# Optimization experiments

Measured on AMD Instinct MI355X. Metric: run time of the kernel, lower is better.

The kernel has to match this reference:

```python
import jax, jax.numpy as jnp
import numpy as np

NUM_HEADS = 16  # matches init_kwargs num_heads


def setup_inputs() -> dict:
    key = jax.random.key(0)
    k0, k1, k2, k3, k4 = jax.random.split(key, 5)
    B, p, C = 8, 64, 1024
    N = p * p
    s = 1.0 / np.sqrt(C).astype(np.float32)
    return {
        "x": jax.random.normal(k0, (B, 3, N, C), jnp.float32),
        "wq": jax.random.normal(k1, (C, C), jnp.float32) * s,
        "wk": jax.random.normal(k2, (C, C), jnp.float32) * s,
        "wv": jax.random.normal(k3, (C, C), jnp.float32) * s,
        "w_proj": jax.random.normal(k4, (C, C), jnp.float32) * s,
        "b_proj": jnp.zeros((C,), jnp.float32),
    }


def reference(x, wq, wk, wv, w_proj, b_proj):
    # x: [B, 3, N, C] triplane tokens, N = p*p
    B, G, N, C = x.shape
    p = int(round(N ** 0.5))
    H = NUM_HEADS
    d = C // H
    scale = d ** -0.5

    xg = x.reshape(B, 3, p, p, C)
    # Linear projections are pointwise, so project each plane element once
    # (the torch code redundantly projects gathered copies; math is identical).
    qh = (xg @ wq.T).reshape(B, 3, p, p, H, d)
    kh = (xg @ wk.T).reshape(B, 3, p, p, H, d)
    vh = (xg @ wv.T).reshape(B, 3, p, p, H, d)

    outs = []
    for i in range(3):  # fixed loop over the 3 planes
        q_i = qh[:, i]                       # [B, a, j, H, d] query pixel (a, j)
        k_yz = kh[:, (i + 1) % 3]            # keys: row a of next plane -> [B, a, k, H, d]
        v_yz = vh[:, (i + 1) % 3]
        k_zx = kh[:, (i + 2) % 3]            # keys: column j of other plane -> [B, k, j, H, d]
        v_zx = vh[:, (i + 2) % 3]
        # scores against the p row-keys and p column-keys (2p keys total, 1 query)
        s1 = jnp.einsum('bajhd,bakhd->bajhk', q_i, k_yz) * scale
        s2 = jnp.einsum('bajhd,bkjhd->bajhk', q_i, k_zx) * scale
        attn = jax.nn.softmax(jnp.concatenate([s1, s2], axis=-1), axis=-1)  # [B,a,j,H,2p]
        a1, a2 = attn[..., :p], attn[..., p:]
        o = (jnp.einsum('bajhk,bakhd->bajhd', a1, v_yz)
             + jnp.einsum('bajhk,bkjhd->bajhd', a2, v_zx))  # [B,a,j,H,d]
        outs.append(o.reshape(B, N, C))
    # torch buffer is filled in [plane, B, N] order then reinterpreted as [B,3,N];
    # replicate that reshape quirk faithfully.
    out = jnp.stack(outs, axis=0)            # [3, B, N, C]
    out = out @ w_proj.T + b_proj
    return out.reshape(B, 3, N, C)
```

## Files before the change

kernel.cpp:

```cpp
#include <hip/hip_runtime.h>
#include <hip/hip_bf16.h>
#include <stdint.h>
#include <type_traits>

typedef __hip_bfloat16 hbf16;
typedef short bf16x8 __attribute__((ext_vector_type(8)));
typedef float f32x4 __attribute__((ext_vector_type(4)));

#define MFMA16(a, b, c) __builtin_amdgcn_mfma_f32_16x16x32_bf16((a), (b), (c), 0, 0, 0)

__device__ __forceinline__ void gload_lds16(const void* g, void* l) {
  __builtin_amdgcn_global_load_lds(
      (const __attribute__((address_space(1))) void*)g,
      (__attribute__((address_space(3))) void*)l, 16, 0, 0);
}

__device__ __forceinline__ float b2f(unsigned short u) {
  union { unsigned int u32; float f; } cv;
  cv.u32 = ((unsigned int)u) << 16;
  return cv.f;
}
__device__ __forceinline__ unsigned short f2b(float f) {
  hbf16 h = __float2bfloat16(f);
  return __builtin_bit_cast(unsigned short, h);
}

__device__ __forceinline__ int swz(int row, int col) {
  return row * 64 + (col ^ ((row & 7) << 3));
}

__global__ __launch_bounds__(256) void cvt_f32_bf16(
    const float* __restrict__ src, unsigned short* __restrict__ dst, long long n)
{
  const long long i0 = ((long long)blockIdx.x * 256 + threadIdx.x) * 8;
  const long long stride = (long long)gridDim.x * 2048;
  for (long long i = i0; i < n; i += stride) {
    const float4 a = *(const float4*)(src + i);
    const float4 b = *(const float4*)(src + i + 4);
    bf16x8 o;
    o[0] = (short)f2b(a.x); o[1] = (short)f2b(a.y);
    o[2] = (short)f2b(a.z); o[3] = (short)f2b(a.w);
    o[4] = (short)f2b(b.x); o[5] = (short)f2b(b.y);
    o[6] = (short)f2b(b.z); o[7] = (short)f2b(b.w);
    *(bf16x8*)(dst + i) = o;
  }
}

template <typename OutT>
__global__ __launch_bounds__(512, 2) void gemm_bt(
    const unsigned short* __restrict__ A,
    const unsigned short* __restrict__ W,
    const float* __restrict__ bias,
    OutT* __restrict__ C,
    int M, int N, int K)
{
  __shared__ __attribute__((aligned(16))) unsigned short As[4][8192];
  __shared__ __attribute__((aligned(16))) unsigned short Bs[4][8192];

  const int tid   = threadIdx.x;
  const int lane  = tid & 63;
  const int w     = tid >> 6;
  const int wr128 = (w >> 2) * 128;
  const int wn64  = (w & 3) * 64;
  const int lr    = lane & 15;
  const int lg    = lane >> 4;
  const int wofs  = w * 512;

  const int nwg     = gridDim.x;
  const int bx      = blockIdx.x;
  const int logical = (bx & 7) * (nwg >> 3) + (bx >> 3);
  const int colsN   = N >> 8;
  const int tileM   = logical / colsN;
  const int tileN   = logical - tileM * colsN;
  const size_t rowBase = (size_t)tileM * 256;
  const int    colBase = tileN * 256;

  const int sRow   = tid >> 2;
  const int sChunk = (tid & 3) ^ ((tid >> 3) & 3);
  const unsigned short* Ag0 = A + (rowBase + sRow) * (size_t)K + sChunk * 8;
  const unsigned short* Ag1 = Ag0 + (size_t)128 * K;
  const unsigned short* Wg0 = W + ((size_t)colBase + sRow) * K + sChunk * 8;
  const unsigned short* Wg1 = Wg0 + (size_t)128 * K;

  f32x4 acc[8][4] = {};

  const int nt = K >> 5;

#pragma unroll
  for (int p = 0; p < 3; ++p) {
    const size_t ke = (size_t)p * 32;
    gload_lds16(Ag0 + ke, &As[p][0] + wofs);
    gload_lds16(Ag1 + ke, &As[p][0] + wofs + 4096);
    gload_lds16(Wg0 + ke, &Bs[p][0] + wofs);
    gload_lds16(Wg1 + ke, &Bs[p][0] + wofs + 4096);
  }

#define GITER(T, VM, STG)                                                     \
  do {                                                                        \
    asm volatile("s_waitcnt vmcnt(" VM ")" ::: "memory");                     \
    __builtin_amdgcn_s_barrier();                                             \
    __builtin_amdgcn_sched_barrier(0);                                        \
    const unsigned short* asb = &As[(T) & 3][0];                              \
    const unsigned short* bsb = &Bs[(T) & 3][0];                              \
    bf16x8 af[8];                                                             \
    bf16x8 bfv[4];                                                            \
    _Pragma("unroll")                                                         \
    for (int mi = 0; mi < 8; ++mi) {                                          \
      const int row = wr128 + mi * 16 + lr;                                   \
      af[mi] = *(const bf16x8*)(asb + row * 32 + (lg ^ ((row >> 1) & 3)) * 8);\
    }                                                                         \
    _Pragma("unroll")                                                         \
    for (int ni = 0; ni < 4; ++ni) {                                          \
      const int row = wn64 + ni * 16 + lr;                                    \
      bfv[ni] = *(const bf16x8*)(bsb + row * 32 + (lg ^ ((row >> 1) & 3)) * 8);\
    }                                                                         \
    if (STG) {                                                                \
      const size_t ke = (size_t)((T) + 3) * 32;                               \
      const int nb = ((T) + 3) & 3;                                           \
      gload_lds16(Ag0 + ke, &As[nb][0] + wofs);                               \
      gload_lds16(Ag1 + ke, &As[nb][0] + wofs + 4096);                        \
      gload_lds16(Wg0 + ke, &Bs[nb][0] + wofs);                               \
      gload_lds16(Wg1 + ke, &Bs[nb][0] + wofs + 4096);                        \
    }                                                                         \
    __builtin_amdgcn_s_setprio(1);                                            \
    _Pragma("unroll")                                                         \
    for (int mi = 0; mi < 8; ++mi)                                            \
      _Pragma("unroll")                                                       \
      for (int ni = 0; ni < 4; ++ni)                                          \
        acc[mi][ni] = MFMA16(af[mi], bfv[ni], acc[mi][ni]);                   \
    __builtin_amdgcn_s_setprio(0);                                            \
  } while (0)

  for (int t = 0; t < nt - 3; ++t) GITER(t, "8", true);
  GITER(nt - 3, "8", false);
  GITER(nt - 2, "4", false);
  GITER(nt - 1, "0", false);
#undef GITER

  const int rg = lg * 4;
#pragma unroll
  for (int ni = 0; ni < 4; ++ni) {
    const int col = colBase + wn64 + ni * 16 + lr;
    const float bv = bias ? bias[col] : 0.0f;
#pragma unroll
    for (int mi = 0; mi < 8; ++mi) {
#pragma unroll
      for (int r = 0; r < 4; ++r) {
        const size_t row = rowBase + wr128 + mi * 16 + rg + r;
        const float val = acc[mi][ni][r] + bv;
        if constexpr (std::is_same_v<OutT, float>) C[row * (size_t)N + col] = val;
        else                                       C[row * (size_t)N + col] = f2b(val);
      }
    }
  }
}

__global__ __launch_bounds__(256) void attn_yz(
    const unsigned short* __restrict__ Q,
    const unsigned short* __restrict__ Kx,
    const unsigned short* __restrict__ Vx,
    unsigned short* __restrict__ O1,
    float* __restrict__ m1s, float* __restrict__ l1s)
{
  __shared__ __attribute__((aligned(16))) unsigned short Qs[4096], Ks[4096], Vs[4096], Ps[4096];

  const int bid = blockIdx.x;
  const int h = bid & 15;
  const int a = (bid >> 4) & 63;
  const int b = (bid >> 10) & 7;
  const int i = bid >> 13;
  const int i1 = (i + 1) % 3;

  const size_t qoff = ((size_t)((b * 3 + i) * 4096 + a * 64)) * 1024 + h * 64;
  const size_t koff = ((size_t)((b * 3 + i1) * 4096 + a * 64)) * 1024 + h * 64;

  const int tid = threadIdx.x;
#pragma unroll
  for (int it = 0; it < 2; ++it) {
    const int idx = it * 2048 + tid * 8;
    const int row = idx >> 6, col = idx & 63;
    const int d = swz(row, col);
    *(bf16x8*)&Qs[d] = *(const bf16x8*)(Q + qoff + (size_t)row * 1024 + col);
    *(bf16x8*)&Ks[d] = *(const bf16x8*)(Kx + koff + (size_t)row * 1024 + col);
    *(bf16x8*)&Vs[d] = *(const bf16x8*)(Vx + koff + (size_t)row * 1024 + col);
  }
  __syncthreads();

  const int lane = tid & 63;
  const int w  = tid >> 6;
  const int lr = lane & 15;
  const int lg = lane >> 4;

  f32x4 sa[4] = {};
  {
    const bf16x8 aq0 = *(const bf16x8*)&Qs[swz(w * 16 + lr, lg * 8)];
    const bf16x8 aq1 = *(const bf16x8*)&Qs[swz(w * 16 + lr, 32 + lg * 8)];
#pragma unroll
    for (int nf = 0; nf < 4; ++nf) {
      const bf16x8 bk0 = *(const bf16x8*)&Ks[swz(nf * 16 + lr, lg * 8)];
      const bf16x8 bk1 = *(const bf16x8*)&Ks[swz(nf * 16 + lr, 32 + lg * 8)];
      sa[nf] = MFMA16(aq0, bk0, sa[nf]);
      sa[nf] = MFMA16(aq1, bk1, sa[nf]);
    }
  }

  const float scale = 0.125f;
  float m[4], ls[4];
#pragma unroll
  for (int r = 0; r < 4; ++r) {
#pragma unroll
    for (int nf = 0; nf < 4; ++nf) sa[nf][r] *= scale;
    float v = fmaxf(fmaxf(sa[0][r], sa[1][r]), fmaxf(sa[2][r], sa[3][r]));
    v = fmaxf(v, __shfl_xor(v, 1));
    v = fmaxf(v, __shfl_xor(v, 2));
    v = fmaxf(v, __shfl_xor(v, 4));
    v = fmaxf(v, __shfl_xor(v, 8));
    m[r] = v;
    float s = 0.0f;
#pragma unroll
    for (int nf = 0; nf < 4; ++nf) { const float p = __expf(sa[nf][r] - v); sa[nf][r] = p; s += p; }
    s += __shfl_xor(s, 1);
    s += __shfl_xor(s, 2);
    s += __shfl_xor(s, 4);
    s += __shfl_xor(s, 8);
    ls[r] = s;
  }

#pragma unroll
  for (int nf = 0; nf < 4; ++nf)
#pragma unroll
    for (int r = 0; r < 4; ++r)
      Ps[swz(w * 16 + lg * 4 + r, nf * 16 + lr)] = f2b(sa[nf][r]);

  if (lr == 0) {
    const size_t sb = ((size_t)(i * 8 + b) * 16 + h) * 4096 + a * 64 + w * 16 + lg * 4;
#pragma unroll
    for (int r = 0; r < 4; ++r) { m1s[sb + r] = m[r]; l1s[sb + r] = ls[r]; }
  }
  __syncthreads();

  f32x4 oa[4] = {};
#pragma unroll
  for (int ks = 0; ks < 2; ++ks) {
    const bf16x8 ap = *(const bf16x8*)&Ps[swz(w * 16 + lr, ks * 32 + lg * 8)];
#pragma unroll
    for (int df = 0; df < 4; ++df) {
      bf16x8 bv;
#pragma unroll
      for (int e = 0; e < 8; ++e)
        bv[e] = (short)Vs[swz(ks * 32 + lg * 8 + e, df * 16 + lr)];
      oa[df] = MFMA16(ap, bv, oa[df]);
    }
  }

  const size_t ob = ((size_t)(i * 8 + b) * 4096 + a * 64) * 1024 + h * 64;
#pragma unroll
  for (int df = 0; df < 4; ++df)
#pragma unroll
    for (int r = 0; r < 4; ++r)
      O1[ob + (size_t)(w * 16 + lg * 4 + r) * 1024 + df * 16 + lr] = f2b(oa[df][r]);
}

__global__ __launch_bounds__(256) void attn_zx(
    const unsigned short* __restrict__ Q,
    const unsigned short* __restrict__ Kx,
    const unsigned short* __restrict__ Vx,
    unsigned short* __restrict__ O1,
    const float* __restrict__ m1s, const float* __restrict__ l1s)
{
  __shared__ __attribute__((aligned(16))) unsigned short Qs[4096], Ks[4096], Vs[4096], Ps[4096];

  const int bid = blockIdx.x;
  const int j = bid & 63;
  const int h = (bid >> 6) & 15;
  const int b = (bid >> 10) & 7;
  const int i = bid >> 13;
  const int i2 = (i + 2) % 3;

  const size_t qoff = ((size_t)(b * 3 + i) * 4096 + j) * 1024 + h * 64;
  const size_t koff = ((size_t)(b * 3 + i2) * 4096 + j) * 1024 + h * 64;
  const size_t rstride = 65536;

  const int tid = threadIdx.x;
#pragma unroll
  for (int it = 0; it < 2; ++it) {
    const int idx = it * 2048 + tid * 8;
    const int row = idx >> 6, col = idx & 63;
    const int d = swz(row, col);
    *(bf16x8*)&Qs[d] = *(const bf16x8*)(Q + qoff + (size_t)row * rstride + col);
    *(bf16x8*)&Ks[d] = *(const bf16x8*)(Kx + koff + (size_t)row * rstride + col);
    *(bf16x8*)&Vs[d] = *(const bf16x8*)(Vx + koff + (size_t)row * rstride + col);
  }
  __syncthreads();

  const int lane = tid & 63;
  const int w  = tid >> 6;
  const int lr = lane & 15;
  const int lg = lane >> 4;

  f32x4 sa[4] = {};
  {
    const bf16x8 aq0 = *(const bf16x8*)&Qs[swz(w * 16 + lr, lg * 8)];
    const bf16x8 aq1 = *(const bf16x8*)&Qs[swz(w * 16 + lr, 32 + lg * 8)];
#pragma unroll
    for (int nf = 0; nf < 4; ++nf) {
      const bf16x8 bk0 = *(const bf16x8*)&Ks[swz(nf * 16 + lr, lg * 8)];
      const bf16x8 bk1 = *(const bf16x8*)&Ks[swz(nf * 16 + lr, 32 + lg * 8)];
      sa[nf] = MFMA16(aq0, bk0, sa[nf]);
      sa[nf] = MFMA16(aq1, bk1, sa[nf]);
    }
  }

  const float scale = 0.125f;
  float m[4], ls[4];
#pragma unroll
  for (int r = 0; r < 4; ++r) {
#pragma unroll
    for (int nf = 0; nf < 4; ++nf) sa[nf][r] *= scale;
    float v = fmaxf(fmaxf(sa[0][r], sa[1][r]), fmaxf(sa[2][r], sa[3][r]));
    v = fmaxf(v, __shfl_xor(v, 1));
    v = fmaxf(v, __shfl_xor(v, 2));
    v = fmaxf(v, __shfl_xor(v, 4));
    v = fmaxf(v, __shfl_xor(v, 8));
    m[r] = v;
    float s = 0.0f;
#pragma unroll
    for (int nf = 0; nf < 4; ++nf) { const float p = __expf(sa[nf][r] - v); sa[nf][r] = p; s += p; }
    s += __shfl_xor(s, 1);
    s += __shfl_xor(s, 2);
    s += __shfl_xor(s, 4);
    s += __shfl_xor(s, 8);
    ls[r] = s;
  }

  float c1[4], c2[4], rden[4];
  const size_t sb = ((size_t)(i * 8 + b) * 16 + h) * 4096 + j;
#pragma unroll
  for (int r = 0; r < 4; ++r) {
    const int arow = w * 16 + lg * 4 + r;
    const float mm1 = m1s[sb + (size_t)arow * 64];
    const float ll1 = l1s[sb + (size_t)arow * 64];
    const float mm = fmaxf(mm1, m[r]);
    const float e1 = __expf(mm1 - mm);
    const float e2 = __expf(m[r] - mm);
    c1[r] = e1; c2[r] = e2;
    rden[r] = 1.0f / (e1 * ll1 + e2 * ls[r]);
  }

#pragma unroll
  for (int nf = 0; nf < 4; ++nf)
#pragma unroll
    for (int r = 0; r < 4; ++r)
      Ps[swz(w * 16 + lg * 4 + r, nf * 16 + lr)] = f2b(sa[nf][r]);
  __syncthreads();

  f32x4 oa[4] = {};
#pragma unroll
  for (int ks = 0; ks < 2; ++ks) {
    const bf16x8 ap = *(const bf16x8*)&Ps[swz(w * 16 + lr, ks * 32 + lg * 8)];
#pragma unroll
    for (int df = 0; df < 4; ++df) {
      bf16x8 bv;
#pragma unroll
      for (int e = 0; e < 8; ++e)
        bv[e] = (short)Vs[swz(ks * 32 + lg * 8 + e, df * 16 + lr)];
      oa[df] = MFMA16(ap, bv, oa[df]);
    }
  }

  const size_t ob = ((size_t)(i * 8 + b) * 4096 + j) * 1024 + h * 64;
#pragma unroll
  for (int df = 0; df < 4; ++df)
#pragma unroll
    for (int r = 0; r < 4; ++r) {
      const size_t addr = ob + (size_t)(w * 16 + lg * 4 + r) * rstride + df * 16 + lr;
      const float o1v = b2f(O1[addr]);
      O1[addr] = f2b((c1[r] * o1v + c2[r] * oa[df][r]) * rden[r]);
    }
}

extern "C" void kernel_launch(void* const* d_in, const int* in_sizes, int n_in,
                              void* d_out, int out_size, void* d_ws, size_t ws_size,
                              hipStream_t stream)
{
  const float* x  = (const float*)d_in[0];
  const float* wq = (const float*)d_in[1];
  const float* wk = (const float*)d_in[2];
  const float* wv = (const float*)d_in[3];
  const float* wp = (const float*)d_in[4];
  const float* bp = (const float*)d_in[5];

  const int M = 98304, N = 1024, K = 1024;
  const size_t SLAB = 201326592ull;
  const size_t STAT = 6291456ull;

  char* ws = (char*)d_ws;
  unsigned short* xb  = (unsigned short*)(ws);
  unsigned short* Kb  = (unsigned short*)(ws + SLAB);
  unsigned short* Vb  = (unsigned short*)(ws + 2 * SLAB);
  float* m1s          = (float*)(ws + 3 * SLAB);
  float* l1s          = (float*)(ws + 3 * SLAB + STAT);
  unsigned short* wqb = (unsigned short*)(ws + 3 * SLAB + 2 * STAT);
  unsigned short* wkb = wqb + 1048576;
  unsigned short* wvb = wkb + 1048576;
  unsigned short* wpb = wvb + 1048576;
  unsigned short* Qb  = (unsigned short*)d_out;
  unsigned short* O1  = xb;

  dim3 blk(256);
  cvt_f32_bf16<<<dim3(4096), blk, 0, stream>>>(x,  xb,  (long long)M * 1024);
  cvt_f32_bf16<<<dim3(512),  blk, 0, stream>>>(wq, wqb, 1048576);
  cvt_f32_bf16<<<dim3(512),  blk, 0, stream>>>(wk, wkb, 1048576);
  cvt_f32_bf16<<<dim3(512),  blk, 0, stream>>>(wv, wvb, 1048576);
  cvt_f32_bf16<<<dim3(512),  blk, 0, stream>>>(wp, wpb, 1048576);

  dim3 gg((M / 256) * (N / 256));
  dim3 gblk(512);
  gemm_bt<unsigned short><<<gg, gblk, 0, stream>>>(xb, wqb, (const float*)nullptr, Qb, M, N, K);
  gemm_bt<unsigned short><<<gg, gblk, 0, stream>>>(xb, wkb, (const float*)nullptr, Kb, M, N, K);
  gemm_bt<unsigned short><<<gg, gblk, 0, stream>>>(xb, wvb, (const float*)nullptr, Vb, M, N, K);
  attn_yz<<<dim3(24576), blk, 0, stream>>>(Qb, Kb, Vb, O1, m1s, l1s);
  attn_zx<<<dim3(24576), blk, 0, stream>>>(Qb, Kb, Vb, O1, m1s, l1s);
  gemm_bt<float><<<gg, gblk, 0, stream>>>(O1, wpb, bp, (float*)d_out, M, N, K);
}
```

Before: 1.583 ms.

## Load GEMM weight operand directly into registers, triple-buffer only A in LDS

The bf16 GEMM no longer stages the weight (B) tile through LDS. Each wave now loads its four B fragments straight from global memory into registers, double-buffered in registers one k-step ahead. The A tile stays in LDS, with the 4-stage ring cut to a 3-stage ring prefetched two steps ahead, and the s_setprio hints around the MFMA block are removed. This is meant to shrink LDS use and remove the LDS writes and reads for B. In exchange, waves that share a column block fetch the same weights twice, and the global load latency for B is hidden by only one iteration.

Measured after the change: 1.986 ms. 1.26x slower.

```diff
diff --git a/kernel.cpp b/kernel.cpp
--- a/kernel.cpp
+++ b/kernel.cpp
@@ -54,8 +54,7 @@
     OutT* __restrict__ C,
     int M, int N, int K)
 {
-  __shared__ __attribute__((aligned(16))) unsigned short As[4][8192];
-  __shared__ __attribute__((aligned(16))) unsigned short Bs[4][8192];
+  __shared__ __attribute__((aligned(16))) unsigned short As[3][8192];
 
   const int tid   = threadIdx.x;
   const int lane  = tid & 63;
@@ -79,62 +78,66 @@
   const int sChunk = (tid & 3) ^ ((tid >> 3) & 3);
   const unsigned short* Ag0 = A + (rowBase + sRow) * (size_t)K + sChunk * 8;
   const unsigned short* Ag1 = Ag0 + (size_t)128 * K;
-  const unsigned short* Wg0 = W + ((size_t)colBase + sRow) * K + sChunk * 8;
-  const unsigned short* Wg1 = Wg0 + (size_t)128 * K;
+
+  const unsigned short* Wr0 = W + ((size_t)colBase + wn64 +  0 + lr) * K + lg * 8;
+  const unsigned short* Wr1 = W + ((size_t)colBase + wn64 + 16 + lr) * K + lg * 8;
+  const unsigned short* Wr2 = W + ((size_t)colBase + wn64 + 32 + lr) * K + lg * 8;
+  const unsigned short* Wr3 = W + ((size_t)colBase + wn64 + 48 + lr) * K + lg * 8;
 
   f32x4 acc[8][4] = {};
-
   const int nt = K >> 5;
 
-#pragma unroll
-  for (int p = 0; p < 3; ++p) {
-    const size_t ke = (size_t)p * 32;
-    gload_lds16(Ag0 + ke, &As[p][0] + wofs);
-    gload_lds16(Ag1 + ke, &As[p][0] + wofs + 4096);
-    gload_lds16(Wg0 + ke, &Bs[p][0] + wofs);
-    gload_lds16(Wg1 + ke, &Bs[p][0] + wofs + 4096);
-  }
-
-#define GITER(T, VM, STG)                                                     \
+  bf16x8 bA0, bA1, bA2, bA3, bB0, bB1, bB2, bB3;
+
+  gload_lds16(Ag0, &As[0][0] + wofs);
+  gload_lds16(Ag1, &As[0][0] + wofs + 4096);
+  bA0 = *(const bf16x8*)(Wr0);
+  bA1 = *(const bf16x8*)(Wr1);
+  bA2 = *(const bf16x8*)(Wr2);
+  bA3 = *(const bf16x8*)(Wr3);
+  gload_lds16(Ag0 + 32, &As[1][0] + wofs);
+  gload_lds16(Ag1 + 32, &As[1][0] + wofs + 4096);
+
+#define GITER(T, BC0, BC1, BC2, BC3, BN0, BN1, BN2, BN3, VM)                  \
   do {                                                                        \
     asm volatile("s_waitcnt vmcnt(" VM ")" ::: "memory");                     \
     __builtin_amdgcn_s_barrier();                                             \
     __builtin_amdgcn_sched_barrier(0);                                        \
-    const unsigned short* asb = &As[(T) & 3][0];                              \
-    const unsigned short* bsb = &Bs[(T) & 3][0];                              \
+    if ((T) + 1 < nt) {                                                       \
+      const int ko = ((T) + 1) * 32;                                          \
+      BN0 = *(const bf16x8*)(Wr0 + ko);                                       \
+      BN1 = *(const bf16x8*)(Wr1 + ko);                                       \
+      BN2 = *(const bf16x8*)(Wr2 + ko);                                       \
+      BN3 = *(const bf16x8*)(Wr3 + ko);                                       \
+    }                                                                         \
+    if ((T) + 2 < nt) {                                                       \
+      const int wb = ((T) + 2) % 3;                                           \
+      const size_t ke = (size_t)((T) + 2) * 32;                               \
+      gload_lds16(Ag0 + ke, &As[wb][0] + wofs);                               \
+      gload_lds16(Ag1 + ke, &As[wb][0] + wofs + 4096);                        \
+    }                                                                         \
+    const unsigned short* asb = &As[(T) % 3][0];                              \
     bf16x8 af[8];                                                             \
-    bf16x8 bfv[4];                                                            \
     _Pragma("unroll")                                                         \
     for (int mi = 0; mi < 8; ++mi) {                                          \
       const int row = wr128 + mi * 16 + lr;                                   \
       af[mi] = *(const bf16x8*)(asb + row * 32 + (lg ^ ((row >> 1) & 3)) * 8);\
     }                                                                         \
     _Pragma("unroll")                                                         \
-    for (int ni = 0; ni < 4; ++ni) {                                          \
-      const int row = wn64 + ni * 16 + lr;                                    \
-      bfv[ni] = *(const bf16x8*)(bsb + row * 32 + (lg ^ ((row >> 1) & 3)) * 8);\
+    for (int mi = 0; mi < 8; ++mi) {                                          \
+      acc[mi][0] = MFMA16(af[mi], BC0, acc[mi][0]);                           \
+      acc[mi][1] = MFMA16(af[mi], BC1, acc[mi][1]);                           \
+      acc[mi][2] = MFMA16(af[mi], BC2, acc[mi][2]);                           \
+      acc[mi][3] = MFMA16(af[mi], BC3, acc[mi][3]);                           \
     }                                                                         \
-    if (STG) {                                                                \
-      const size_t ke = (size_t)((T) + 3) * 32;                               \
-      const int nb = ((T) + 3) & 3;                                           \
-      gload_lds16(Ag0 + ke, &As[nb][0] + wofs);                               \
-      gload_lds16(Ag1 + ke, &As[nb][0] + wofs + 4096);                        \
-      gload_lds16(Wg0 + ke, &Bs[nb][0] + wofs);                               \
-      gload_lds16(Wg1 + ke, &Bs[nb][0] + wofs + 4096);                        \
-    }                                                                         \
-    __builtin_amdgcn_s_setprio(1);                                            \
-    _Pragma("unroll")                                                         \
-    for (int mi = 0; mi < 8; ++mi)                                            \
-      _Pragma("unroll")                                                       \
-      for (int ni = 0; ni < 4; ++ni)                                          \
-        acc[mi][ni] = MFMA16(af[mi], bfv[ni], acc[mi][ni]);                   \
-    __builtin_amdgcn_s_setprio(0);                                            \
   } while (0)
 
-  for (int t = 0; t < nt - 3; ++t) GITER(t, "8", true);
-  GITER(nt - 3, "8", false);
-  GITER(nt - 2, "4", false);
-  GITER(nt - 1, "0", false);
+  for (int t = 0; t < nt - 2; t += 2) {
+    GITER(t,     bA0, bA1, bA2, bA3, bB0, bB1, bB2, bB3, "2");
+    GITER(t + 1, bB0, bB1, bB2, bB3, bA0, bA1, bA2, bA3, "2");
+  }
+  GITER(nt - 2, bA0, bA1, bA2, bA3, bB0, bB1, bB2, bB3, "2");
+  GITER(nt - 1, bB0, bB1, bB2, bB3, bA0, bA1, bA2, bA3, "0");
 #undef GITER
 
   const int rg = lg * 4;
```

## Shrink GEMM tile to 256x128, triple-buffer LDS, stage epilogue through LDS

Applied to the files above, without the earlier changes.

The projection GEMM tile shrinks from 256x256 to 256x128, with 8 warps each computing 64x64 and a 3-stage LDS ring instead of 4. Launch bounds move to 4 blocks per CU to raise occupancy. The epilogue writes accumulators to LDS and then issues coalesced 16-byte global stores instead of scattered scalar stores. In exchange each output element gets less reuse, more A traffic is reloaded, the prefetch distance is shorter, and the setprio hints are removed.

New measurement: 1.445 ms. 8.7% less time.

```diff
diff --git a/kernel.cpp b/kernel.cpp
--- a/kernel.cpp
+++ b/kernel.cpp
@@ -6,6 +6,7 @@
 typedef __hip_bfloat16 hbf16;
 typedef short bf16x8 __attribute__((ext_vector_type(8)));
 typedef float f32x4 __attribute__((ext_vector_type(4)));
+typedef unsigned int u32x4 __attribute__((ext_vector_type(4)));
 
 #define MFMA16(a, b, c) __builtin_amdgcn_mfma_f32_16x16x32_bf16((a), (b), (c), 0, 0, 0)
 
@@ -47,52 +48,48 @@
 }
 
 template <typename OutT>
-__global__ __launch_bounds__(512, 2) void gemm_bt(
+__global__ __launch_bounds__(512, 4) void gemm_bt(
     const unsigned short* __restrict__ A,
     const unsigned short* __restrict__ W,
     const float* __restrict__ bias,
     OutT* __restrict__ C,
     int M, int N, int K)
 {
-  __shared__ __attribute__((aligned(16))) unsigned short As[4][8192];
-  __shared__ __attribute__((aligned(16))) unsigned short Bs[4][8192];
-
-  const int tid   = threadIdx.x;
-  const int lane  = tid & 63;
-  const int w     = tid >> 6;
-  const int wr128 = (w >> 2) * 128;
-  const int wn64  = (w & 3) * 64;
-  const int lr    = lane & 15;
-  const int lg    = lane >> 4;
-  const int wofs  = w * 512;
+  __shared__ __attribute__((aligned(16))) unsigned short Sm[36864];
+
+  const int tid  = threadIdx.x;
+  const int lane = tid & 63;
+  const int w    = tid >> 6;
+  const int wr64 = (w >> 1) * 64;
+  const int wc64 = (w & 1) * 64;
+  const int lr   = lane & 15;
+  const int lg   = lane >> 4;
+  const int wofs = w * 512;
 
   const int nwg     = gridDim.x;
   const int bx      = blockIdx.x;
   const int logical = (bx & 7) * (nwg >> 3) + (bx >> 3);
-  const int colsN   = N >> 8;
+  const int colsN   = N >> 7;
   const int tileM   = logical / colsN;
   const int tileN   = logical - tileM * colsN;
   const size_t rowBase = (size_t)tileM * 256;
-  const int    colBase = tileN * 256;
+  const int    colBase = tileN * 128;
 
   const int sRow   = tid >> 2;
   const int sChunk = (tid & 3) ^ ((tid >> 3) & 3);
   const unsigned short* Ag0 = A + (rowBase + sRow) * (size_t)K + sChunk * 8;
   const unsigned short* Ag1 = Ag0 + (size_t)128 * K;
   const unsigned short* Wg0 = W + ((size_t)colBase + sRow) * K + sChunk * 8;
-  const unsigned short* Wg1 = Wg0 + (size_t)128 * K;
-
-  f32x4 acc[8][4] = {};
-
+
+  f32x4 acc[4][4] = {};
   const int nt = K >> 5;
 
 #pragma unroll
-  for (int p = 0; p < 3; ++p) {
+  for (int p = 0; p < 2; ++p) {
     const size_t ke = (size_t)p * 32;
-    gload_lds16(Ag0 + ke, &As[p][0] + wofs);
-    gload_lds16(Ag1 + ke, &As[p][0] + wofs + 4096);
-    gload_lds16(Wg0 + ke, &Bs[p][0] + wofs);
-    gload_lds16(Wg1 + ke, &Bs[p][0] + wofs + 4096);
+    gload_lds16(Ag0 + ke, Sm + p * 8192 + wofs);
+    gload_lds16(Ag1 + ke, Sm + p * 8192 + 4096 + wofs);
+    gload_lds16(Wg0 + ke, Sm + 24576 + p * 4096 + wofs);
   }
 
 #define GITER(T, VM, STG)                                                     \
@@ -100,56 +97,91 @@
     asm volatile("s_waitcnt vmcnt(" VM ")" ::: "memory");                     \
     __builtin_amdgcn_s_barrier();                                             \
     __builtin_amdgcn_sched_barrier(0);                                        \
-    const unsigned short* asb = &As[(T) & 3][0];                              \
-    const unsigned short* bsb = &Bs[(T) & 3][0];                              \
-    bf16x8 af[8];                                                             \
-    bf16x8 bfv[4];                                                            \
+    if (STG) {                                                                \
+      const int nb = ((T) + 2) % 3;                                           \
+      const size_t ke = (size_t)((T) + 2) * 32;                               \
+      gload_lds16(Ag0 + ke, Sm + nb * 8192 + wofs);                           \
+      gload_lds16(Ag1 + ke, Sm + nb * 8192 + 4096 + wofs);                    \
+      gload_lds16(Wg0 + ke, Sm + 24576 + nb * 4096 + wofs);                   \
+    }                                                                         \
+    const unsigned short* asb = Sm + ((T) % 3) * 8192;                        \
+    const unsigned short* bsb = Sm + 24576 + ((T) % 3) * 4096;                \
+    bf16x8 af[4], bfv[4];                                                     \
     _Pragma("unroll")                                                         \
-    for (int mi = 0; mi < 8; ++mi) {                                          \
-      const int row = wr128 + mi * 16 + lr;                                   \
+    for (int mi = 0; mi < 4; ++mi) {                                          \
+      const int row = wr64 + mi * 16 + lr;                                    \
       af[mi] = *(const bf16x8*)(asb + row * 32 + (lg ^ ((row >> 1) & 3)) * 8);\
     }                                                                         \
     _Pragma("unroll")                                                         \
     for (int ni = 0; ni < 4; ++ni) {                                          \
-      const int row = wn64 + ni * 16 + lr;                                    \
+      const int row = wc64 + ni * 16 + lr;                                    \
       bfv[ni] = *(const bf16x8*)(bsb + row * 32 + (lg ^ ((row >> 1) & 3)) * 8);\
     }                                                                         \
-    if (STG) {                                                                \
-      const size_t ke = (size_t)((T) + 3) * 32;                               \
-      const int nb = ((T) + 3) & 3;                                           \
-      gload_lds16(Ag0 + ke, &As[nb][0] + wofs);                               \
-      gload_lds16(Ag1 + ke, &As[nb][0] + wofs + 4096);                        \
-      gload_lds16(Wg0 + ke, &Bs[nb][0] + wofs);                               \
-      gload_lds16(Wg1 + ke, &Bs[nb][0] + wofs + 4096);                        \
-    }                                                                         \
-    __builtin_amdgcn_s_setprio(1);                                            \
     _Pragma("unroll")                                                         \
-    for (int mi = 0; mi < 8; ++mi)                                            \
+    for (int mi = 0; mi < 4; ++mi)                                            \
       _Pragma("unroll")                                                       \
       for (int ni = 0; ni < 4; ++ni)                                          \
         acc[mi][ni] = MFMA16(af[mi], bfv[ni], acc[mi][ni]);                   \
-    __builtin_amdgcn_s_setprio(0);                                            \
   } while (0)
 
-  for (int t = 0; t < nt - 3; ++t) GITER(t, "8", true);
-  GITER(nt - 3, "8", false);
-  GITER(nt - 2, "4", false);
+  for (int t = 0; t < nt - 2; ++t) GITER(t, "3", true);
+  GITER(nt - 2, "3", false);
   GITER(nt - 1, "0", false);
 #undef GITER
 
-  const int rg = lg * 4;
-#pragma unroll
-  for (int ni = 0; ni < 4; ++ni) {
-    const int col = colBase + wn64 + ni * 16 + lr;
-    const float bv = bias ? bias[col] : 0.0f;
-#pragma unroll
-    for (int mi = 0; mi < 8; ++mi) {
-#pragma unroll
-      for (int r = 0; r < 4; ++r) {
-        const size_t row = rowBase + wr128 + mi * 16 + rg + r;
-        const float val = acc[mi][ni][r] + bv;
-        if constexpr (std::is_same_v<OutT, float>) C[row * (size_t)N + col] = val;
-        else                                       C[row * (size_t)N + col] = f2b(val);
+  __syncthreads();
+
+  float bv[4];
+#pragma unroll
+  for (int ni = 0; ni < 4; ++ni)
+    bv[ni] = bias ? bias[colBase + wc64 + ni * 16 + lr] : 0.0f;
+
+  const size_t R0 = rowBase + wr64;
+  const int    C0 = colBase + wc64;
+
+#pragma unroll
+  for (int batch = 0; batch < 2; ++batch) {
+    if constexpr (std::is_same_v<OutT, float>) {
+      float* reg = (float*)(void*)Sm + w * 2048;
+#pragma unroll
+      for (int mi2 = 0; mi2 < 2; ++mi2) {
+        const int mi = batch * 2 + mi2;
+#pragma unroll
+        for (int ni = 0; ni < 4; ++ni)
+#pragma unroll
+          for (int r = 0; r < 4; ++r)
+            reg[(mi2 * 16 + lg * 4 + r) * 64 + ni * 16 + lr] =
+                acc[mi][ni][r] + bv[ni];
+      }
+      asm volatile("s_waitcnt lgkmcnt(0)" ::: "memory");
+      __builtin_amdgcn_sched_barrier(0);
+#pragma unroll
+      for (int it = 0; it < 8; ++it) {
+        const int ch  = it * 64 + lane;
+        const int row = ch >> 4, cc = ch & 15;
+        const float4 v = *(const float4*)(reg + row * 64 + cc * 4);
+        *(float4*)((float*)C + (R0 + batch * 32 + row) * (size_t)N + C0 + cc * 4) = v;
+      }
+    } else {
+      unsigned short* reg = Sm + w * 2048;
+#pragma unroll
+      for (int mi2 = 0; mi2 < 2; ++mi2) {
+        const int mi = batch * 2 + mi2;
+#pragma unroll
+        for (int ni = 0; ni < 4; ++ni)
+#pragma unroll
+          for (int r = 0; r < 4; ++r)
+            reg[(mi2 * 16 + lg * 4 + r) * 64 + ni * 16 + lr] =
+                f2b(acc[mi][ni][r] + bv[ni]);
+      }
+      asm volatile("s_waitcnt lgkmcnt(0)" ::: "memory");
+      __builtin_amdgcn_sched_barrier(0);
+#pragma unroll
+      for (int it = 0; it < 4; ++it) {
+        const int ch  = it * 64 + lane;
+        const int row = ch >> 3, cc = ch & 7;
+        const u32x4 v = *(const u32x4*)(reg + row * 64 + cc * 8);
+        *(u32x4*)((unsigned short*)C + (R0 + batch * 32 + row) * (size_t)N + C0 + cc * 8) = v;
       }
     }
   }
@@ -414,7 +446,7 @@
   cvt_f32_bf16<<<dim3(512),  blk, 0, stream>>>(wv, wvb, 1048576);
   cvt_f32_bf16<<<dim3(512),  blk, 0, stream>>>(wp, wpb, 1048576);
 
-  dim3 gg((M / 256) * (N / 256));
+  dim3 gg((M / 256) * (N / 128));
   dim3 gblk(512);
   gemm_bt<unsigned short><<<gg, gblk, 0, stream>>>(xb, wqb, (const float*)nullptr, Qb, M, N, K);
   gemm_bt<unsigned short><<<gg, gblk, 0, stream>>>(xb, wkb, (const float*)nullptr, Kb, M, N, K);
```
